# Kernel tuning notes

Hardware: AMD Instinct MI355X
Metric: run time of the kernel (lower is better)

Reference implementation:

```python
import jax, jax.numpy as jnp
import numpy as np

N = 20000   # nodes
E = 320000  # edges (before self-loops)
HID = 64    # hidden_dim
H = 4       # attention heads
C = HID     # per-head channels (concat=False -> mean over heads)
CDIM = 8    # contrastive_dim
NEG_SLOPE = 0.2


def setup_inputs() -> dict:
    key = jax.random.key(0)
    ks = jax.random.split(key, 32)
    g = lambda k, shape: (jax.random.normal(k, shape, jnp.float32) * 0.05)
    inp = {
        "x": jax.random.normal(ks[0], (N, 8), jnp.float32),
        "edge_index": jax.random.randint(ks[1], (2, E), 0, N, jnp.int64),
        # lc_encode MLP: 8 -> 32 -> HID
        "W_enc1": g(ks[2], (8, 32)),  "b_enc1": jnp.zeros((32,), jnp.float32),
        "W_enc2": g(ks[3], (32, HID)), "b_enc2": jnp.zeros((HID,), jnp.float32),
        # three GATConv layers: lin (HID -> H*C, no bias), att_src/att_dst (H, C), bias (C,)
        "W_g1": g(ks[4], (HID, H * C)), "as1": g(ks[5], (H, C)), "ad1": g(ks[6], (H, C)), "bg1": jnp.zeros((C,), jnp.float32),
        "W_g2": g(ks[7], (HID, H * C)), "as2": g(ks[8], (H, C)), "ad2": g(ks[9], (H, C)), "bg2": jnp.zeros((C,), jnp.float32),
        "W_g3": g(ks[10], (HID, H * C)), "as3": g(ks[11], (H, C)), "ad3": g(ks[12], (H, C)), "bg3": jnp.zeros((C,), jnp.float32),
        # output MLP: HID -> 64 -> 32 -> CDIM (dropout inactive at eval)
        "W_o1": g(ks[13], (HID, 64)), "b_o1": jnp.zeros((64,), jnp.float32),
        "W_o2": g(ks[14], (64, 32)),  "b_o2": jnp.zeros((32,), jnp.float32),
        "W_o3": g(ks[15], (32, CDIM)), "b_o3": jnp.zeros((CDIM,), jnp.float32),
    }
    return inp


def gat_conv(x, src, dst, n, W, att_src, att_dst, bias):
    # PyG GATConv, heads=H, concat=False (mean over heads), eval mode (no dropout)
    h = (x @ W).reshape(n, H, C)                       # [N,H,C]
    a_src = jnp.einsum('nhc,hc->nh', h, att_src)        # [N,H]
    a_dst = jnp.einsum('nhc,hc->nh', h, att_dst)        # [N,H]
    logits = jax.nn.leaky_relu(a_src[src] + a_dst[dst], NEG_SLOPE)  # [Etot,H]
    m = jax.ops.segment_max(logits, dst, num_segments=n)            # segment softmax (stable)
    e = jnp.exp(logits - m[dst])
    denom = jax.ops.segment_sum(e, dst, num_segments=n)
    alpha = e / (denom[dst] + 1e-16)                    # [Etot,H]
    msg = h[src] * alpha[:, :, None]                    # [Etot,H,C]
    out = jax.ops.segment_sum(msg, dst, num_segments=n) # [N,H,C]
    return out.mean(axis=1) + bias                      # concat=False -> head mean


def reference(x, edge_index, W_enc1, b_enc1, W_enc2, b_enc2,
              W_g1, as1, ad1, bg1, W_g2, as2, ad2, bg2, W_g3, as3, ad3, bg3,
              W_o1, b_o1, W_o2, b_o2, W_o3, b_o3):
    n = x.shape[0]
    loops = jnp.arange(n, dtype=edge_index.dtype)       # GATConv add_self_loops=True
    src = jnp.concatenate([edge_index[0], loops])
    dst = jnp.concatenate([edge_index[1], loops])

    h = jax.nn.elu(jax.nn.elu(x @ W_enc1 + b_enc1) @ W_enc2 + b_enc2)
    h1 = gat_conv(h, src, dst, n, W_g1, as1, ad1, bg1) + h
    h2 = gat_conv(h1, src, dst, n, W_g2, as2, ad2, bg2) + h1
    h3 = gat_conv(h2, src, dst, n, W_g3, as3, ad3, bg3) + h2

    o = jax.nn.elu(h3 @ W_o1 + b_o1)
    o = jax.nn.elu(o @ W_o2 + b_o2)
    return o @ W_o3 + b_o3
```

## Files before the change

kernel.cpp:

```cpp
#include <hip/hip_runtime.h>
#include <cstdint>
#include <cstddef>

#define NEG_SLOPE 0.2f

__device__ __forceinline__ float elu_f(float x) {
    return x > 0.f ? x : expm1f(x);
}

__global__ __launch_bounds__(256) void prep_kernel(
    const int* __restrict__ ei,
    const float* __restrict__ W0, const float* __restrict__ as0, const float* __restrict__ ad0,
    const float* __restrict__ W1, const float* __restrict__ as1, const float* __restrict__ ad1,
    const float* __restrict__ W2, const float* __restrict__ as2, const float* __restrict__ ad2,
    int* __restrict__ cnt, int* __restrict__ ready, int* __restrict__ flag,
    float* __restrict__ vfold, int n) {
    const int b = blockIdx.x, t = threadIdx.x;
    if (b < 79) {
        const int i = b * 256 + t;
        if (i < n) cnt[i] = 0;
        if (b == 0) {
            if (t < 128) ready[t] = 0;
            if (t == 0) {
                int acc = 0;
#pragma unroll
                for (int k = 0; k < 8; ++k) acc |= ei[2 * k + 1];
                flag[0] = (acc == 0) ? 1 : 0;
            }
        }
        return;
    }
    const int e = (b - 79) * 256 + t;
    if (e >= 1536) return;
    const int l = e >> 9, rem = e & 511;
    const int k = rem >> 3, j = rem & 7, h = j & 3;
    const float* W   = (l == 0) ? W0  : (l == 1) ? W1  : W2;
    const float* as_ = (l == 0) ? as0 : (l == 1) ? as1 : as2;
    const float* ad_ = (l == 0) ? ad0 : (l == 1) ? ad1 : ad2;
    const float* av = (j < 4) ? as_ : ad_;
    const float* wr = W + k * 256 + h * 64;
    const float* ar = av + h * 64;
    float s = 0.f;
#pragma unroll 8
    for (int cc = 0; cc < 64; ++cc) s += wr[cc] * ar[cc];
    vfold[l * 512 + k * 8 + j] = s;
}

__global__ void count_kernel(const int* __restrict__ ei, const int* __restrict__ flag,
                             int E, int Etot, int* __restrict__ cnt) {
    int e = blockIdx.x * blockDim.x + threadIdx.x;
    if (e >= Etot) return;
    int d;
    if (e < E) d = flag[0] ? ei[2 * (size_t)(E + e)] : ei[E + e];
    else       d = e - E;
    atomicAdd(&cnt[d], 1);
}

#define SCAN_B 256
__global__ __launch_bounds__(256) void scan_onepass_kernel(
    const int* __restrict__ cnt, int* __restrict__ ready,
    int* __restrict__ rowptr, int* __restrict__ cursor, int n) {
    __shared__ int sd[SCAN_B];
    __shared__ int sred[128];
    __shared__ int s_pref;
    const int b = blockIdx.x, t = threadIdx.x;
    const int g = b * SCAN_B + t;
    const int v = (g < n) ? cnt[g] : 0;
    sd[t] = v;
    __syncthreads();
    for (int off = 1; off < SCAN_B; off <<= 1) {
        int add = (t >= off) ? sd[t - off] : 0;
        __syncthreads();
        sd[t] += add;
        __syncthreads();
    }
    if (t == SCAN_B - 1) atomicExch(&ready[b], sd[SCAN_B - 1] + 1);
    if (t < 128) {
        int pv = 0;
        if (t < b) {
            do { pv = atomicAdd(&ready[t], 0); __builtin_amdgcn_s_sleep(1); } while (pv == 0);
            pv -= 1;
        }
        sred[t] = pv;
    }
    __syncthreads();
    if (t == 0) {
        int s = 0;
#pragma unroll 8
        for (int i = 0; i < 128; ++i) s += sred[i];
        s_pref = s;
    }
    __syncthreads();
    const int pre = s_pref;
    if (g < n) {
        const int e = pre + sd[t];
        rowptr[g + 1] = e;
        cursor[g] = e - v;
        if (g == 0) rowptr[0] = 0;
    }
}

__global__ void fill_kernel(const int* __restrict__ ei, const int* __restrict__ flag,
                            int E, int Etot, int* __restrict__ cursor,
                            int* __restrict__ col) {
    int e = blockIdx.x * blockDim.x + threadIdx.x;
    if (e >= Etot) return;
    int s, d;
    if (e < E) {
        if (flag[0]) { s = ei[2 * (size_t)e]; d = ei[2 * (size_t)(E + e)]; }
        else         { s = ei[e];             d = ei[E + e]; }
    } else {
        s = d = e - E;
    }
    int pos = atomicAdd(&cursor[d], 1);
    col[pos] = s;
}

__global__ __launch_bounds__(256) void encoder_kernel(
    const float* __restrict__ x,
    const float* __restrict__ W1, const float* __restrict__ b1,
    const float* __restrict__ W2, const float* __restrict__ b2,
    const float* __restrict__ vfold0,
    float* __restrict__ h0, float* __restrict__ asrc, float* __restrict__ adst,
    int n_nodes) {
    __shared__ float vsd[512];
    const int t = threadIdx.x;
    if (t < 128) *(float4*)(vsd + t * 4) = *(const float4*)(vfold0 + t * 4);
    __syncthreads();
    const int i = blockIdx.x * blockDim.x + t;
    if (i >= n_nodes) return;
    const float4* xp = (const float4*)(x + (size_t)i * 8);
    float4 x0 = xp[0], x1 = xp[1];
    float xi[8] = {x0.x, x0.y, x0.z, x0.w, x1.x, x1.y, x1.z, x1.w};
    float h1[32];
#pragma unroll
    for (int j = 0; j < 32; ++j) {
        float a = b1[j];
#pragma unroll
        for (int k = 0; k < 8; ++k) a += xi[k] * W1[k * 32 + j];
        h1[j] = elu_f(a);
    }
    float* dst = h0 + (size_t)i * 64;
    float adot[8];
#pragma unroll
    for (int jj = 0; jj < 8; ++jj) adot[jj] = 0.f;
    for (int j = 0; j < 64; ++j) {
        float a = b2[j];
#pragma unroll
        for (int k = 0; k < 32; ++k) a += h1[k] * W2[k * 64 + j];
        a = elu_f(a);
        dst[j] = a;
#pragma unroll
        for (int jj = 0; jj < 8; ++jj) adot[jj] += a * vsd[j * 8 + jj];
    }
#pragma unroll
    for (int h = 0; h < 4; ++h) {
        asrc[i * 4 + h] = adot[h];
        adst[i * 4 + h] = adot[4 + h];
    }
}

__global__ __launch_bounds__(256) void gat_agg_kernel(
    const float* __restrict__ bin, const float* __restrict__ asrc,
    const float* __restrict__ adst, const int* __restrict__ rowptr,
    const int* __restrict__ col, float* __restrict__ g, int n_nodes) {
    const int grp = threadIdx.x >> 4;
    const int q = threadIdx.x & 15;
    const int n = blockIdx.x * 16 + grp;
    if (n >= n_nodes) return;
    const float4 ad4 = *(const float4*)(adst + (size_t)n * 4);
    const int start = rowptr[n], end = rowptr[n + 1];

    float acc[4][4];
#pragma unroll
    for (int h = 0; h < 4; ++h)
#pragma unroll
        for (int z = 0; z < 4; ++z) acc[h][z] = 0.f;
    float4 den4 = make_float4(0.f, 0.f, 0.f, 0.f);

    for (int base = start; base < end; base += 16) {
        const int cnt = min(16, end - base);
        int c = 0;
        float4 w4 = make_float4(0.f, 0.f, 0.f, 0.f);
        if (base + q < end) {
            c = col[base + q];
            const float4 av = *(const float4*)(asrc + (size_t)c * 4);
            float l0 = av.x + ad4.x; l0 = l0 > 0.f ? l0 : NEG_SLOPE * l0;
            float l1 = av.y + ad4.y; l1 = l1 > 0.f ? l1 : NEG_SLOPE * l1;
            float l2 = av.z + ad4.z; l2 = l2 > 0.f ? l2 : NEG_SLOPE * l2;
            float l3 = av.w + ad4.w; l3 = l3 > 0.f ? l3 : NEG_SLOPE * l3;
            w4.x = __expf(fminf(l0, 60.f));
            w4.y = __expf(fminf(l1, 60.f));
            w4.z = __expf(fminf(l2, 60.f));
            w4.w = __expf(fminf(l3, 60.f));
            den4.x += w4.x; den4.y += w4.y; den4.z += w4.z; den4.w += w4.w;
        }
        int j = 0;
        for (; j + 4 <= cnt; j += 4) {
#pragma unroll
            for (int u = 0; u < 4; ++u) {
                const int s = __shfl(c, j + u, 16);
                const float4 hv = *(const float4*)(bin + (size_t)s * 64 + q * 4);
                const float wx = __shfl(w4.x, j + u, 16);
                const float wy = __shfl(w4.y, j + u, 16);
                const float wz = __shfl(w4.z, j + u, 16);
                const float ww = __shfl(w4.w, j + u, 16);
                acc[0][0] += wx * hv.x; acc[0][1] += wx * hv.y;
                acc[0][2] += wx * hv.z; acc[0][3] += wx * hv.w;
                acc[1][0] += wy * hv.x; acc[1][1] += wy * hv.y;
                acc[1][2] += wy * hv.z; acc[1][3] += wy * hv.w;
                acc[2][0] += wz * hv.x; acc[2][1] += wz * hv.y;
                acc[2][2] += wz * hv.z; acc[2][3] += wz * hv.w;
                acc[3][0] += ww * hv.x; acc[3][1] += ww * hv.y;
                acc[3][2] += ww * hv.z; acc[3][3] += ww * hv.w;
            }
        }
        for (; j < cnt; ++j) {
            const int s = __shfl(c, j, 16);
            const float4 hv = *(const float4*)(bin + (size_t)s * 64 + q * 4);
            const float wx = __shfl(w4.x, j, 16);
            const float wy = __shfl(w4.y, j, 16);
            const float wz = __shfl(w4.z, j, 16);
            const float ww = __shfl(w4.w, j, 16);
            acc[0][0] += wx * hv.x; acc[0][1] += wx * hv.y;
            acc[0][2] += wx * hv.z; acc[0][3] += wx * hv.w;
            acc[1][0] += wy * hv.x; acc[1][1] += wy * hv.y;
            acc[1][2] += wy * hv.z; acc[1][3] += wy * hv.w;
            acc[2][0] += wz * hv.x; acc[2][1] += wz * hv.y;
            acc[2][2] += wz * hv.z; acc[2][3] += wz * hv.w;
            acc[3][0] += ww * hv.x; acc[3][1] += ww * hv.y;
            acc[3][2] += ww * hv.z; acc[3][3] += ww * hv.w;
        }
    }
#pragma unroll
    for (int off = 1; off < 16; off <<= 1) {
        den4.x += __shfl_xor(den4.x, off, 16);
        den4.y += __shfl_xor(den4.y, off, 16);
        den4.z += __shfl_xor(den4.z, off, 16);
        den4.w += __shfl_xor(den4.w, off, 16);
    }
    const float i0 = 1.f / (den4.x + 1e-16f);
    const float i1 = 1.f / (den4.y + 1e-16f);
    const float i2 = 1.f / (den4.z + 1e-16f);
    const float i3 = 1.f / (den4.w + 1e-16f);
    float* gr = g + (size_t)n * 256 + q * 4;
    *(float4*)(gr +   0) = make_float4(acc[0][0]*i0, acc[0][1]*i0, acc[0][2]*i0, acc[0][3]*i0);
    *(float4*)(gr +  64) = make_float4(acc[1][0]*i1, acc[1][1]*i1, acc[1][2]*i1, acc[1][3]*i1);
    *(float4*)(gr + 128) = make_float4(acc[2][0]*i2, acc[2][1]*i2, acc[2][2]*i2, acc[2][3]*i2);
    *(float4*)(gr + 192) = make_float4(acc[3][0]*i3, acc[3][1]*i3, acc[3][2]*i3, acc[3][3]*i3);
}

#define GSTR 132
__global__ __launch_bounds__(256) void gat_post_kernel(
    const float* __restrict__ g, const float* __restrict__ W,
    const float* __restrict__ bias, const float* __restrict__ xin,
    const float* __restrict__ vfold_next, int has_next,
    float* __restrict__ out, float* __restrict__ asrc, float* __restrict__ adst,
    const float* __restrict__ Wm1, const float* __restrict__ bm1,
    const float* __restrict__ Wm2, const float* __restrict__ bm2,
    const float* __restrict__ Wm3, const float* __restrict__ bm3,
    float* __restrict__ mlp_out, int n_nodes) {
    __shared__ float gS[64 * GSTR];
    __shared__ float Wp[128 * 64];
    __shared__ float vN[512];
    const int t = threadIdx.x;
    const int n0 = blockIdx.x * 64;
    const int cg = t & 7;
    const int ng = t >> 3;

    if (has_next && t < 128) *(float4*)(vN + t * 4) = *(const float4*)(vfold_next + t * 4);

    float acc[2][8];
#pragma unroll
    for (int i = 0; i < 2; ++i)
#pragma unroll
        for (int qq = 0; qq < 8; ++qq) acc[i][qq] = 0.f;

    for (int slab = 0; slab < 2; ++slab) {
        __syncthreads();
#pragma unroll
        for (int j = 0; j < 8; ++j) {
            const int idx = j * 256 + t;
            const int nl = idx >> 5;
            const int c4 = idx & 31;
            float4 v = make_float4(0.f, 0.f, 0.f, 0.f);
            if (n0 + nl < n_nodes)
                v = *(const float4*)(g + (size_t)(n0 + nl) * 256 + slab * 128 + c4 * 4);
            *(float4*)(gS + nl * GSTR + c4 * 4) = v;
        }
#pragma unroll
        for (int j = 0; j < 8; ++j) {
            const int f4 = j * 256 + t;
            const int kl = f4 >> 4;
            const int kap = slab * 128 + kl;
            const int h = kap >> 6, kk = kap & 63;
            const int c = (f4 & 15) * 4;
            *(float4*)(Wp + kl * 64 + c) = *(const float4*)(W + kk * 256 + h * 64 + c);
        }
        __syncthreads();
#pragma unroll 4
        for (int kl = 0; kl < 128; ++kl) {
            const float a0 = gS[(ng * 2 + 0) * GSTR + kl];
            const float a1 = gS[(ng * 2 + 1) * GSTR + kl];
            const float4 b0 = *(const float4*)(Wp + kl * 64 + cg * 8);
            const float4 b1 = *(const float4*)(Wp + kl * 64 + cg * 8 + 4);
            acc[0][0] += a0 * b0.x; acc[0][1] += a0 * b0.y;
            acc[0][2] += a0 * b0.z; acc[0][3] += a0 * b0.w;
            acc[0][4] += a0 * b1.x; acc[0][5] += a0 * b1.y;
            acc[0][6] += a0 * b1.z; acc[0][7] += a0 * b1.w;
            acc[1][0] += a1 * b0.x; acc[1][1] += a1 * b0.y;
            acc[1][2] += a1 * b0.z; acc[1][3] += a1 * b0.w;
            acc[1][4] += a1 * b1.x; acc[1][5] += a1 * b1.y;
            acc[1][6] += a1 * b1.z; acc[1][7] += a1 * b1.w;
        }
    }

    const int c0 = cg * 8;
    const float4 bb0 = *(const float4*)(bias + c0);
    const float4 bb1 = *(const float4*)(bias + c0 + 4);
    float o[2][8];
#pragma unroll
    for (int i = 0; i < 2; ++i) {
        const int n = n0 + ng * 2 + i;
        if (n < n_nodes) {
            const float4 x0 = *(const float4*)(xin + (size_t)n * 64 + c0);
            const float4 x1 = *(const float4*)(xin + (size_t)n * 64 + c0 + 4);
            o[i][0] = 0.25f * acc[i][0] + bb0.x + x0.x;
            o[i][1] = 0.25f * acc[i][1] + bb0.y + x0.y;
            o[i][2] = 0.25f * acc[i][2] + bb0.z + x0.z;
            o[i][3] = 0.25f * acc[i][3] + bb0.w + x0.w;
            o[i][4] = 0.25f * acc[i][4] + bb1.x + x1.x;
            o[i][5] = 0.25f * acc[i][5] + bb1.y + x1.y;
            o[i][6] = 0.25f * acc[i][6] + bb1.z + x1.z;
            o[i][7] = 0.25f * acc[i][7] + bb1.w + x1.w;
            if (has_next) {
                *(float4*)(out + (size_t)n * 64 + c0) =
                    make_float4(o[i][0], o[i][1], o[i][2], o[i][3]);
                *(float4*)(out + (size_t)n * 64 + c0 + 4) =
                    make_float4(o[i][4], o[i][5], o[i][6], o[i][7]);
            }
        } else {
#pragma unroll
            for (int qq = 0; qq < 8; ++qq) o[i][qq] = 0.f;
        }
    }

    if (has_next) {
        float pj[2][8];
#pragma unroll
        for (int i = 0; i < 2; ++i)
#pragma unroll
            for (int jj = 0; jj < 8; ++jj) pj[i][jj] = 0.f;
#pragma unroll
        for (int cidx = 0; cidx < 8; ++cidx) {
#pragma unroll
            for (int jj = 0; jj < 8; ++jj) {
                const float vv = vN[(c0 + cidx) * 8 + jj];
                pj[0][jj] += o[0][cidx] * vv;
                pj[1][jj] += o[1][cidx] * vv;
            }
        }
#pragma unroll
        for (int off = 1; off < 8; off <<= 1) {
#pragma unroll
            for (int i = 0; i < 2; ++i)
#pragma unroll
                for (int jj = 0; jj < 8; ++jj)
                    pj[i][jj] += __shfl_xor(pj[i][jj], off);
        }
        if (cg == 0) {
#pragma unroll
            for (int i = 0; i < 2; ++i) {
                const int n = n0 + ng * 2 + i;
                if (n < n_nodes) {
#pragma unroll
                    for (int h = 0; h < 4; ++h) {
                        asrc[n * 4 + h] = pj[i][h];
                        adst[n * 4 + h] = pj[i][4 + h];
                    }
                }
            }
        }
        return;
    }

    __syncthreads();
#pragma unroll
    for (int i = 0; i < 2; ++i) {
        const int nl = ng * 2 + i;
        *(float4*)(gS + nl * GSTR + c0)     = make_float4(o[i][0], o[i][1], o[i][2], o[i][3]);
        *(float4*)(gS + nl * GSTR + c0 + 4) = make_float4(o[i][4], o[i][5], o[i][6], o[i][7]);
    }
    {
        const int f4 = t;
#pragma unroll
        for (int j = 0; j < 4; ++j)
            *(float4*)(Wp + (j * 256 + t) * 4) = *(const float4*)(Wm1 + (j * 256 + t) * 4);
#pragma unroll
        for (int j = 0; j < 2; ++j)
            *(float4*)(Wp + 4096 + (j * 256 + t) * 4) = *(const float4*)(Wm2 + (j * 256 + t) * 4);
        if (t < 64) vN[t] = bm1[t];
        else if (t < 96) vN[t] = bm2[t - 64];
        else if (t < 104) vN[t] = bm3[t - 96];
        if (t < 256) vN[104 + t] = Wm3[t];
        (void)f4;
    }
    __syncthreads();
    {
        float a1[2][8];
#pragma unroll
        for (int i = 0; i < 2; ++i)
#pragma unroll
            for (int qq = 0; qq < 8; ++qq) a1[i][qq] = vN[c0 + qq];
#pragma unroll 4
        for (int k = 0; k < 64; ++k) {
            const float h0 = gS[(ng * 2 + 0) * GSTR + k];
            const float h1v = gS[(ng * 2 + 1) * GSTR + k];
            const float4 w0 = *(const float4*)(Wp + k * 64 + c0);
            const float4 w1 = *(const float4*)(Wp + k * 64 + c0 + 4);
            a1[0][0] += h0 * w0.x; a1[0][1] += h0 * w0.y;
            a1[0][2] += h0 * w0.z; a1[0][3] += h0 * w0.w;
            a1[0][4] += h0 * w1.x; a1[0][5] += h0 * w1.y;
            a1[0][6] += h0 * w1.z; a1[0][7] += h0 * w1.w;
            a1[1][0] += h1v * w0.x; a1[1][1] += h1v * w0.y;
            a1[1][2] += h1v * w0.z; a1[1][3] += h1v * w0.w;
            a1[1][4] += h1v * w1.x; a1[1][5] += h1v * w1.y;
            a1[1][6] += h1v * w1.z; a1[1][7] += h1v * w1.w;
        }
#pragma unroll
        for (int i = 0; i < 2; ++i) {
            const int nl = ng * 2 + i;
            float4 v0 = make_float4(elu_f(a1[i][0]), elu_f(a1[i][1]), elu_f(a1[i][2]), elu_f(a1[i][3]));
            float4 v1 = make_float4(elu_f(a1[i][4]), elu_f(a1[i][5]), elu_f(a1[i][6]), elu_f(a1[i][7]));
            *(float4*)(gS + nl * GSTR + 64 + c0)     = v0;
            *(float4*)(gS + nl * GSTR + 64 + c0 + 4) = v1;
        }
    }
    __syncthreads();
    {
        const int cg4 = t & 3;
        const int nn = t >> 2;
        const int cc0 = cg4 * 8;
        float a2[8];
#pragma unroll
        for (int qq = 0; qq < 8; ++qq) a2[qq] = vN[64 + cc0 + qq];
#pragma unroll 4
        for (int j = 0; j < 64; ++j) {
            const float ov = gS[nn * GSTR + 64 + j];
            const float4 w0 = *(const float4*)(Wp + 4096 + j * 32 + cc0);
            const float4 w1 = *(const float4*)(Wp + 4096 + j * 32 + cc0 + 4);
            a2[0] += ov * w0.x; a2[1] += ov * w0.y;
            a2[2] += ov * w0.z; a2[3] += ov * w0.w;
            a2[4] += ov * w1.x; a2[5] += ov * w1.y;
            a2[6] += ov * w1.z; a2[7] += ov * w1.w;
        }
        __syncthreads();
        *(float4*)(gS + nn * GSTR + cc0)     = make_float4(elu_f(a2[0]), elu_f(a2[1]), elu_f(a2[2]), elu_f(a2[3]));
        *(float4*)(gS + nn * GSTR + cc0 + 4) = make_float4(elu_f(a2[4]), elu_f(a2[5]), elu_f(a2[6]), elu_f(a2[7]));
    }
    __syncthreads();
    {
        const int c3 = t & 7;
        const int nq = t >> 3;
#pragma unroll
        for (int i = 0; i < 2; ++i) {
            const int nl = nq * 2 + i;
            const int n = n0 + nl;
            if (n >= n_nodes) continue;
            float a3 = vN[96 + c3];
#pragma unroll 4
            for (int j = 0; j < 32; ++j)
                a3 += gS[nl * GSTR + j] * vN[104 + j * 8 + c3];
            mlp_out[(size_t)n * 8 + c3] = a3;
        }
    }
}

extern "C" void kernel_launch(void* const* d_in, const int* in_sizes, int n_in,
                              void* d_out, int out_size, void* d_ws, size_t ws_size,
                              hipStream_t stream) {
    const float* x     = (const float*)d_in[0];
    const int*   ei    = (const int*)d_in[1];
    const float* Wenc1 = (const float*)d_in[2];
    const float* benc1 = (const float*)d_in[3];
    const float* Wenc2 = (const float*)d_in[4];
    const float* benc2 = (const float*)d_in[5];
    const float* Wg[3]  = {(const float*)d_in[6],  (const float*)d_in[10], (const float*)d_in[14]};
    const float* as_[3] = {(const float*)d_in[7],  (const float*)d_in[11], (const float*)d_in[15]};
    const float* ad_[3] = {(const float*)d_in[8],  (const float*)d_in[12], (const float*)d_in[16]};
    const float* bg[3]  = {(const float*)d_in[9],  (const float*)d_in[13], (const float*)d_in[17]};
    const float* Wo1 = (const float*)d_in[18];
    const float* bo1 = (const float*)d_in[19];
    const float* Wo2 = (const float*)d_in[20];
    const float* bo2 = (const float*)d_in[21];
    const float* Wo3 = (const float*)d_in[22];
    const float* bo3 = (const float*)d_in[23];

    const int N = in_sizes[0] / 8;
    const int E = in_sizes[1] / 2;
    const int Etot = E + N;
    const int nblk = (N + SCAN_B - 1) / SCAN_B;

    float* buf0  = (float*)d_ws;
    float* buf1  = buf0 + (size_t)N * 64;
    float* g     = buf1 + (size_t)N * 64;
    float* asrc  = g + (size_t)N * 256;
    float* adst  = asrc + (size_t)N * 4;
    float* vfold = adst + (size_t)N * 4;
    int* rowptr = (int*)(vfold + 3 * 512);
    int* cursor = rowptr + (N + 2);
    int* cnt    = cursor + N;
    int* ready  = cnt + N;
    int* flag   = ready + 128;
    int* col    = flag + 2;

    prep_kernel<<<nblk + 6, 256, 0, stream>>>(ei,
        Wg[0], as_[0], ad_[0], Wg[1], as_[1], ad_[1], Wg[2], as_[2], ad_[2],
        cnt, ready, flag, vfold, N);
    count_kernel<<<(Etot + 255) / 256, 256, 0, stream>>>(ei, flag, E, Etot, cnt);
    scan_onepass_kernel<<<nblk, SCAN_B, 0, stream>>>(cnt, ready, rowptr, cursor, N);
    fill_kernel<<<(Etot + 255) / 256, 256, 0, stream>>>(ei, flag, E, Etot, cursor, col);

    encoder_kernel<<<(N + 255) / 256, 256, 0, stream>>>(x, Wenc1, benc1, Wenc2, benc2,
                                                        vfold, buf0, asrc, adst, N);

    float* bin = buf0;
    float* bout = buf1;
    for (int l = 0; l < 3; ++l) {
        gat_agg_kernel<<<(N + 15) / 16, 256, 0, stream>>>(bin, asrc, adst, rowptr, col,
                                                          g, N);
        const int has_next = (l < 2) ? 1 : 0;
        gat_post_kernel<<<(N + 63) / 64, 256, 0, stream>>>(
            g, Wg[l], bg[l], bin, vfold + (l + 1 < 3 ? (l + 1) * 512 : 0), has_next,
            bout, asrc, adst,
            Wo1, bo1, Wo2, bo2, Wo3, bo3, (float*)d_out, N);
        float* tmp = bin; bin = bout; bout = tmp;
    }
}
```

Before: 305.2 us.

## Restructure encoder as block-tiled shared-memory MLP with 64 nodes per block

The encoder used to give each thread a whole node and read weights from global memory, with scalar stores to the 64-wide output. Now each block stages the weights and inputs in shared memory and handles 64 nodes. Threads cooperatively compute the first layer into a transposed tile, then compute the second layer as a 4x4 register tile, writing float4s. Attention dot products are reduced across threads with shuffles. This aims to cut global weight traffic, register pressure and uncoalesced stores, at the cost of more shared memory per block and more blocks.

```diff
diff --git a/kernel.cpp b/kernel.cpp
--- a/kernel.cpp
+++ b/kernel.cpp
@@ -116,6 +116,7 @@
     col[pos] = s;
 }
 
+#define H1STR 68
 __global__ __launch_bounds__(256) void encoder_kernel(
     const float* __restrict__ x,
     const float* __restrict__ W1, const float* __restrict__ b1,
@@ -123,40 +124,123 @@
     const float* __restrict__ vfold0,
     float* __restrict__ h0, float* __restrict__ asrc, float* __restrict__ adst,
     int n_nodes) {
+    __shared__ float W1s[256];
+    __shared__ float b1s[32];
+    __shared__ float W2s[2048];
+    __shared__ float b2s[64];
     __shared__ float vsd[512];
+    __shared__ float xS[512];
+    __shared__ float h1T[32 * H1STR];
     const int t = threadIdx.x;
+    const int n0 = blockIdx.x * 64;
+    const int rem = n_nodes - n0;
+
+    *(float4*)(W2s + t * 4) = *(const float4*)(W2 + t * 4);
+    *(float4*)(W2s + 1024 + t * 4) = *(const float4*)(W2 + 1024 + t * 4);
+    if (t < 64)  *(float4*)(W1s + t * 4) = *(const float4*)(W1 + t * 4);
+    if (t < 8)   *(float4*)(b1s + t * 4) = *(const float4*)(b1 + t * 4);
+    if (t < 16)  *(float4*)(b2s + t * 4) = *(const float4*)(b2 + t * 4);
     if (t < 128) *(float4*)(vsd + t * 4) = *(const float4*)(vfold0 + t * 4);
-    __syncthreads();
-    const int i = blockIdx.x * blockDim.x + t;
-    if (i >= n_nodes) return;
-    const float4* xp = (const float4*)(x + (size_t)i * 8);
-    float4 x0 = xp[0], x1 = xp[1];
-    float xi[8] = {x0.x, x0.y, x0.z, x0.w, x1.x, x1.y, x1.z, x1.w};
-    float h1[32];
-#pragma unroll
-    for (int j = 0; j < 32; ++j) {
-        float a = b1[j];
-#pragma unroll
-        for (int k = 0; k < 8; ++k) a += xi[k] * W1[k * 32 + j];
-        h1[j] = elu_f(a);
-    }
-    float* dst = h0 + (size_t)i * 64;
-    float adot[8];
-#pragma unroll
-    for (int jj = 0; jj < 8; ++jj) adot[jj] = 0.f;
-    for (int j = 0; j < 64; ++j) {
-        float a = b2[j];
-#pragma unroll
-        for (int k = 0; k < 32; ++k) a += h1[k] * W2[k * 64 + j];
-        a = elu_f(a);
-        dst[j] = a;
-#pragma unroll
-        for (int jj = 0; jj < 8; ++jj) adot[jj] += a * vsd[j * 8 + jj];
-    }
-#pragma unroll
-    for (int h = 0; h < 4; ++h) {
-        asrc[i * 4 + h] = adot[h];
-        adst[i * 4 + h] = adot[4 + h];
+    if (t < 128) {
+        const int fidx = t * 4;
+        float4 v = make_float4(0.f, 0.f, 0.f, 0.f);
+        if (fidx < rem * 8) v = *(const float4*)(x + (size_t)n0 * 8 + fidx);
+        *(float4*)(xS + fidx) = v;
+    }
+    __syncthreads();
+
+    {
+        const int nl = t >> 2;
+        const int j0 = (t & 3) * 8;
+        const float4 xa = *(const float4*)(xS + nl * 8);
+        const float4 xb = *(const float4*)(xS + nl * 8 + 4);
+        const float xk[8] = {xa.x, xa.y, xa.z, xa.w, xb.x, xb.y, xb.z, xb.w};
+        float a[8];
+#pragma unroll
+        for (int u = 0; u < 8; ++u) a[u] = b1s[j0 + u];
+#pragma unroll
+        for (int k = 0; k < 8; ++k) {
+            const float4 w0 = *(const float4*)(W1s + k * 32 + j0);
+            const float4 w1 = *(const float4*)(W1s + k * 32 + j0 + 4);
+            a[0] += xk[k] * w0.x; a[1] += xk[k] * w0.y;
+            a[2] += xk[k] * w0.z; a[3] += xk[k] * w0.w;
+            a[4] += xk[k] * w1.x; a[5] += xk[k] * w1.y;
+            a[6] += xk[k] * w1.z; a[7] += xk[k] * w1.w;
+        }
+#pragma unroll
+        for (int u = 0; u < 8; ++u) h1T[(j0 + u) * H1STR + nl] = elu_f(a[u]);
+    }
+    __syncthreads();
+
+    const int cg = t & 15;
+    const int nq = t >> 4;
+    const int c0 = cg * 4;
+    float acc[4][4];
+#pragma unroll
+    for (int i = 0; i < 4; ++i)
+#pragma unroll
+        for (int c = 0; c < 4; ++c) acc[i][c] = b2s[c0 + c];
+#pragma unroll 8
+    for (int k = 0; k < 32; ++k) {
+        const float4 hv = *(const float4*)(h1T + k * H1STR + nq * 4);
+        const float4 wv = *(const float4*)(W2s + k * 64 + c0);
+        const float hvv[4] = {hv.x, hv.y, hv.z, hv.w};
+#pragma unroll
+        for (int i = 0; i < 4; ++i) {
+            acc[i][0] += hvv[i] * wv.x; acc[i][1] += hvv[i] * wv.y;
+            acc[i][2] += hvv[i] * wv.z; acc[i][3] += hvv[i] * wv.w;
+        }
+    }
+    float o[4][4];
+#pragma unroll
+    for (int i = 0; i < 4; ++i)
+#pragma unroll
+        for (int c = 0; c < 4; ++c) o[i][c] = elu_f(acc[i][c]);
+
+#pragma unroll
+    for (int i = 0; i < 4; ++i) {
+        const int n = n0 + nq * 4 + i;
+        if (n < n_nodes)
+            *(float4*)(h0 + (size_t)n * 64 + c0) =
+                make_float4(o[i][0], o[i][1], o[i][2], o[i][3]);
+    }
+    float ad[4][8];
+#pragma unroll
+    for (int i = 0; i < 4; ++i)
+#pragma unroll
+        for (int jj = 0; jj < 8; ++jj) ad[i][jj] = 0.f;
+#pragma unroll
+    for (int c = 0; c < 4; ++c) {
+        const float4 v0 = *(const float4*)(vsd + (c0 + c) * 8);
+        const float4 v1 = *(const float4*)(vsd + (c0 + c) * 8 + 4);
+#pragma unroll
+        for (int i = 0; i < 4; ++i) {
+            ad[i][0] += o[i][c] * v0.x; ad[i][1] += o[i][c] * v0.y;
+            ad[i][2] += o[i][c] * v0.z; ad[i][3] += o[i][c] * v0.w;
+            ad[i][4] += o[i][c] * v1.x; ad[i][5] += o[i][c] * v1.y;
+            ad[i][6] += o[i][c] * v1.z; ad[i][7] += o[i][c] * v1.w;
+        }
+    }
+#pragma unroll
+    for (int off = 1; off < 16; off <<= 1) {
+#pragma unroll
+        for (int i = 0; i < 4; ++i)
+#pragma unroll
+            for (int jj = 0; jj < 8; ++jj)
+                ad[i][jj] += __shfl_xor(ad[i][jj], off);
+    }
+    if (cg == 0) {
+#pragma unroll
+        for (int i = 0; i < 4; ++i) {
+            const int n = n0 + nq * 4 + i;
+            if (n < n_nodes) {
+#pragma unroll
+                for (int h = 0; h < 4; ++h) {
+                    asrc[n * 4 + h] = ad[i][h];
+                    adst[n * 4 + h] = ad[i][4 + h];
+                }
+            }
+        }
     }
 }
 
@@ -392,7 +476,6 @@
         *(float4*)(gS + nl * GSTR + c0 + 4) = make_float4(o[i][4], o[i][5], o[i][6], o[i][7]);
     }
     {
-        const int f4 = t;
 #pragma unroll
         for (int j = 0; j < 4; ++j)
             *(float4*)(Wp + (j * 256 + t) * 4) = *(const float4*)(Wm1 + (j * 256 + t) * 4);
@@ -402,8 +485,7 @@
         if (t < 64) vN[t] = bm1[t];
         else if (t < 96) vN[t] = bm2[t - 64];
         else if (t < 104) vN[t] = bm3[t - 96];
-        if (t < 256) vN[104 + t] = Wm3[t];
-        (void)f4;
+        vN[104 + t] = Wm3[t];
     }
     __syncthreads();
     {
@@ -521,8 +603,8 @@
     scan_onepass_kernel<<<nblk, SCAN_B, 0, stream>>>(cnt, ready, rowptr, cursor, N);
     fill_kernel<<<(Etot + 255) / 256, 256, 0, stream>>>(ei, flag, E, Etot, cursor, col);
 
-    encoder_kernel<<<(N + 255) / 256, 256, 0, stream>>>(x, Wenc1, benc1, Wenc2, benc2,
-                                                        vfold, buf0, asrc, adst, N);
+    encoder_kernel<<<(N + 63) / 64, 256, 0, stream>>>(x, Wenc1, benc1, Wenc2, benc2,
+                                                      vfold, buf0, asrc, adst, N);
 
     float* bin = buf0;
     float* bout = buf1;
```

New measurement: 287.5 us. 1.06x faster.
